# Performance work log

Hardware: AMD Instinct MI355X
Metric: run time of the kernel (lower is better)

Reference implementation:

```python
import jax, jax.numpy as jnp
import numpy as np

LEAK_RATE = 0.5
SPECTRAL_RADIUS = 0.9
T, IN_DIM, R_DIM, OUT_DIM = 32768, 128, 1024, 64


def setup_inputs() -> dict:
    key = jax.random.key(0)
    k1, k2, k3, k4 = jax.random.split(key, 4)
    input_data = jax.random.normal(k1, (T, IN_DIM), dtype=jnp.float32)
    # reservoir weights with spectral radius normalization (as in __init__)
    W = np.array(jax.random.normal(k2, (R_DIM, R_DIM), dtype=jnp.float32), dtype=np.float64)
    W *= SPECTRAL_RADIUS / np.max(np.abs(np.linalg.eigvals(W)))
    reservoir_weights = jnp.asarray(W, dtype=jnp.float32)
    input_weights = jax.random.normal(k3, (R_DIM, IN_DIM), dtype=jnp.float32)
    output_weights = jax.random.normal(k4, (R_DIM, OUT_DIM), dtype=jnp.float32) * 0.02
    return {
        "input_data": input_data,
        "input_weights": input_weights,
        "reservoir_weights": reservoir_weights,
        "output_weights": output_weights,
    }


def reference(input_data, input_weights, reservoir_weights, output_weights):
    a = jnp.float32(LEAK_RATE)
    # precompute input projection for all timesteps: [T, R]
    u = input_data @ input_weights.T

    def step(s, u_t):
        s_dec = (1.0 - a) * s                      # decayed previous state
        s_new = s_dec + a * jnp.tanh(u_t + reservoir_weights @ s_dec)
        return s_new, s_new

    s0 = jnp.zeros((reservoir_weights.shape[0],), dtype=input_data.dtype)
    _, states = jax.lax.scan(step, s0, u)          # states: [T, R]
    predictions = states @ output_weights          # [T, OUT_DIM]
    return predictions
```

## Files before the change

### kernel.cpp

```cpp
#include <hip/hip_runtime.h>
#include <math.h>


#define G_BLOCKS 32
#define ROWS     32
#define TPB      256
#define T_STEPS  32768
#define R_DIM    1024
#define IN_DIM   128
#define OUT_DIM  64

__global__ __launch_bounds__(TPB, 1)
void esn_scan_kernel(const float* __restrict__ x,
                     const float* __restrict__ Win,
                     const float* __restrict__ W,
                     const float* __restrict__ Wout,
                     float* __restrict__ out,
                     unsigned long long* __restrict__ sbuf)
{
    constexpr float A   = 0.5f;
    constexpr float DEC = 0.5f;

    const int b    = blockIdx.x;
    const int tid  = threadIdx.x;
    const int lane = tid & 63;
    const int wave = tid >> 6;
    const int r    = tid & 31;
    const int kg   = tid >> 5;

    __shared__ float s_dec[R_DIM];
    __shared__ float part[8][ROWS];
    __shared__ float u_lds[2][ROWS];
    __shared__ float s_new_lds[ROWS];
    __shared__ float x_lds[2][IN_DIM];
    __shared__ float win_lds[ROWS * 132];
    __shared__ float wout_lds[ROWS * OUT_DIM];

    float w[128];
    {
        const float* wrow = W + ((size_t)(b * ROWS + r)) * R_DIM + kg * 128;
        #pragma unroll
        for (int j = 0; j < 128; j += 4) {
            const float4 v = *(const float4*)(wrow + j);
            w[j] = v.x; w[j+1] = v.y; w[j+2] = v.z; w[j+3] = v.w;
        }
    }
    for (int i = tid; i < ROWS * IN_DIM; i += TPB) {
        int rr = i >> 7, cc = i & 127;
        win_lds[rr * 132 + cc] = Win[((size_t)(b * ROWS + rr)) * IN_DIM + cc];
    }
    for (int i = tid; i < ROWS * OUT_DIM; i += TPB)
        wout_lds[i] = Wout[(size_t)b * ROWS * OUT_DIM + i];
    for (int i = tid; i < R_DIM; i += TPB) s_dec[i] = 0.0f;
    if (tid < IN_DIM) {
        x_lds[0][tid] = x[tid];
        x_lds[1][tid] = x[IN_DIM + tid];
    }
    __syncthreads();

    if (wave == 1) {
        int rr = lane & 31, kh = lane >> 5;
        float acc = 0.f;
        const float* wl = &win_lds[rr * 132 + kh * 64];
        const float* xl = &x_lds[0][kh * 64];
        #pragma unroll
        for (int i = 0; i < 64; i += 4) {
            float4 wv = *(const float4*)(wl + i);
            float4 xv = *(const float4*)(xl + i);
            acc += wv.x*xv.x + wv.y*xv.y + wv.z*xv.z + wv.w*xv.w;
        }
        acc += __shfl_down(acc, 32);
        if (lane < 32) u_lds[0][rr] = acc;
    }
    __syncthreads();

    for (int t = 0; t < T_STEPS; ++t) {
        {
            float a0 = 0.f, a1 = 0.f, a2 = 0.f, a3 = 0.f;
            const float* sp = &s_dec[kg * 128];
            #pragma unroll
            for (int j = 0; j < 128; j += 4) {
                const float4 sv = *(const float4*)(sp + j);
                a0 += w[j]   * sv.x;
                a1 += w[j+1] * sv.y;
                a2 += w[j+2] * sv.z;
                a3 += w[j+3] * sv.w;
            }
            part[kg][r] = (a0 + a1) + (a2 + a3);
        }
        __syncthreads();

        if (wave == 0) {
            float snew = 0.f;
            if (lane < 32) {
                float tot = 0.f;
                #pragma unroll
                for (int k = 0; k < 8; ++k) tot += part[k][lane];
                const float y  = u_lds[t & 1][lane] + tot;
                const float sd = s_dec[b * ROWS + lane];
                snew = sd + A * tanhf(y);
                s_new_lds[lane] = snew;
                const unsigned long long pkt =
                    ((unsigned long long)(unsigned int)(t + 1) << 32)
                    | (unsigned long long)__float_as_uint(snew);
                __hip_atomic_store(&sbuf[(size_t)(t & 1) * R_DIM + b * ROWS + lane],
                                   pkt, __ATOMIC_RELAXED, __HIP_MEMORY_SCOPE_AGENT);
            }
        } else if (wave == 1 && t + 1 < T_STEPS) {
            const int tpre = (t + 2 < T_STEPS) ? (t + 2) : (T_STEPS - 1);
            const float xv0 = x[(size_t)tpre * IN_DIM + lane];
            const float xv1 = x[(size_t)tpre * IN_DIM + 64 + lane];
            int rr = lane & 31, kh = lane >> 5;
            float acc = 0.f;
            const float* wl = &win_lds[rr * 132 + kh * 64];
            const float* xl = &x_lds[(t + 1) & 1][kh * 64];
            #pragma unroll
            for (int i = 0; i < 64; i += 4) {
                float4 wv = *(const float4*)(wl + i);
                float4 xv = *(const float4*)(xl + i);
                acc += wv.x*xv.x + wv.y*xv.y + wv.z*xv.z + wv.w*xv.w;
            }
            acc += __shfl_down(acc, 32);
            if (lane < 32) u_lds[(t + 1) & 1][rr] = acc;
            x_lds[t & 1][lane]      = xv0;
            x_lds[t & 1][64 + lane] = xv1;
        }
        __syncthreads();

        if (wave == 2) {
            float acc = 0.f;
            #pragma unroll
            for (int rr = 0; rr < 32; ++rr)
                acc += s_new_lds[rr] * wout_lds[rr * OUT_DIM + lane];
            atomicAdd(&out[(size_t)t * OUT_DIM + lane], acc);
        }
        if (t + 1 < T_STEPS) {
            const int want = t + 1;
            unsigned long long v[4];
            const size_t base = (size_t)(t & 1) * R_DIM;
            #pragma unroll
            for (int j = 0; j < 4; ++j)
                v[j] = __hip_atomic_load(&sbuf[base + j * TPB + tid],
                                         __ATOMIC_RELAXED, __HIP_MEMORY_SCOPE_AGENT);
            bool ok;
            do {
                ok = true;
                #pragma unroll
                for (int j = 0; j < 4; ++j) {
                    if ((int)(v[j] >> 32) != want) {
                        ok = false;
                        __builtin_amdgcn_s_sleep(1);
                        v[j] = __hip_atomic_load(&sbuf[base + j * TPB + tid],
                                                 __ATOMIC_RELAXED,
                                                 __HIP_MEMORY_SCOPE_AGENT);
                    }
                }
            } while (!ok);
            #pragma unroll
            for (int j = 0; j < 4; ++j)
                s_dec[j * TPB + tid] = __uint_as_float((unsigned int)v[j]) * DEC;
        }
        __syncthreads();
    }
}

extern "C" void kernel_launch(void* const* d_in, const int* in_sizes, int n_in,
                              void* d_out, int out_size, void* d_ws, size_t ws_size,
                              hipStream_t stream) {
    const float* x    = (const float*)d_in[0];
    const float* Win  = (const float*)d_in[1];
    const float* W    = (const float*)d_in[2];
    const float* Wout = (const float*)d_in[3];
    float* out = (float*)d_out;
    unsigned long long* sbuf = (unsigned long long*)d_ws;

    hipMemsetAsync(d_out, 0, (size_t)out_size * sizeof(float), stream);

    esn_scan_kernel<<<G_BLOCKS, TPB, 0, stream>>>(x, Win, W, Wout, out, sbuf);
}
```

Baseline: 69.05 ms.

## Restructure ESN scan with packed 24-bit state exchange and separate output GEMM

Rewrites the recurrent scan so each thread computes four rows over a 32-wide k-slice, reduced with wave shuffles. The LDS partial-sum stage and one barrier per step go away. State exchange packs two 24-bit-truncated floats with an 8-bit tag into one 64-bit word, halving polling traffic. tanh uses an exp-based approximation, and the decay factor is folded into the weights. The per-step output projection with atomics is replaced by writing all states to workspace and running a separate tiled GEMM afterward. This trades state precision (24-bit mantissa truncation) and extra memory traffic for a shorter per-step critical path.

After: 135.6 ms. 96.4% more time.

```diff
diff --git a/kernel.cpp b/kernel.cpp
--- a/kernel.cpp
+++ b/kernel.cpp
@@ -3,165 +3,229 @@
 
 
 #define G_BLOCKS 32
-#define ROWS     32
 #define TPB      256
 #define T_STEPS  32768
 #define R_DIM    1024
 #define IN_DIM   128
 #define OUT_DIM  64
 
+__device__ __forceinline__ float tanh_fast(float y) {
+    float e = __expf(2.0f * y);
+    return 1.0f - 2.0f / (e + 1.0f);
+}
+
+__device__ __forceinline__ unsigned pack24(float v, unsigned tag) {
+    unsigned bts = __float_as_uint(v);
+    bts = (bts + 0x80u) >> 8;
+    return (tag << 24) | (bts & 0x00FFFFFFu);
+}
+__device__ __forceinline__ float unpack24(unsigned p) {
+    return __uint_as_float(p << 8);
+}
+
 __global__ __launch_bounds__(TPB, 1)
-void esn_scan_kernel(const float* __restrict__ x,
-                     const float* __restrict__ Win,
-                     const float* __restrict__ W,
-                     const float* __restrict__ Wout,
-                     float* __restrict__ out,
-                     unsigned long long* __restrict__ sbuf)
+void esn_scan(const float* __restrict__ x,
+              const float* __restrict__ Win,
+              const float* __restrict__ W,
+              float* __restrict__ states,
+              unsigned long long* __restrict__ sbuf)
 {
-    constexpr float A   = 0.5f;
-    constexpr float DEC = 0.5f;
-
+    constexpr float A = 0.5f, DEC = 0.5f;
     const int b    = blockIdx.x;
     const int tid  = threadIdx.x;
     const int lane = tid & 63;
     const int wave = tid >> 6;
-    const int r    = tid & 31;
-    const int kg   = tid >> 5;
-
-    __shared__ float s_dec[R_DIM];
-    __shared__ float part[8][ROWS];
-    __shared__ float u_lds[2][ROWS];
-    __shared__ float s_new_lds[ROWS];
+    const int c    = tid & 31;
+    const int rset = tid >> 5;
+    const bool is_pub = (c < 2);
+    const int lrow0 = rset * 4 + 2 * c;
+    const int grow0 = b * 32 + lrow0;
+    const int urow  = wave * 8 + (lane >> 3);
+    const int useg  = lane & 7;
+
+    __shared__ float win_lds[32 * 132];
     __shared__ float x_lds[2][IN_DIM];
-    __shared__ float win_lds[ROWS * 132];
-    __shared__ float wout_lds[ROWS * OUT_DIM];
-
-    float w[128];
+    __shared__ float u_lds[2][32];
+
+    float w0[32], w1[32], w2[32], w3[32];
     {
-        const float* wrow = W + ((size_t)(b * ROWS + r)) * R_DIM + kg * 128;
-        #pragma unroll
-        for (int j = 0; j < 128; j += 4) {
-            const float4 v = *(const float4*)(wrow + j);
-            w[j] = v.x; w[j+1] = v.y; w[j+2] = v.z; w[j+3] = v.w;
-        }
-    }
-    for (int i = tid; i < ROWS * IN_DIM; i += TPB) {
+        const float* base = W + (size_t)(b * 32 + rset * 4) * R_DIM + c * 32;
+        #pragma unroll
+        for (int k = 0; k < 32; k += 4) {
+            float4 v0 = *(const float4*)(base + 0 * R_DIM + k);
+            float4 v1 = *(const float4*)(base + 1 * R_DIM + k);
+            float4 v2 = *(const float4*)(base + 2 * R_DIM + k);
+            float4 v3 = *(const float4*)(base + 3 * R_DIM + k);
+            w0[k]=v0.x*DEC; w0[k+1]=v0.y*DEC; w0[k+2]=v0.z*DEC; w0[k+3]=v0.w*DEC;
+            w1[k]=v1.x*DEC; w1[k+1]=v1.y*DEC; w1[k+2]=v1.z*DEC; w1[k+3]=v1.w*DEC;
+            w2[k]=v2.x*DEC; w2[k+1]=v2.y*DEC; w2[k+2]=v2.z*DEC; w2[k+3]=v2.w*DEC;
+            w3[k]=v3.x*DEC; w3[k+1]=v3.y*DEC; w3[k+2]=v3.z*DEC; w3[k+3]=v3.w*DEC;
+        }
+    }
+    for (int i = tid; i < 32 * IN_DIM; i += TPB) {
         int rr = i >> 7, cc = i & 127;
-        win_lds[rr * 132 + cc] = Win[((size_t)(b * ROWS + rr)) * IN_DIM + cc];
-    }
-    for (int i = tid; i < ROWS * OUT_DIM; i += TPB)
-        wout_lds[i] = Wout[(size_t)b * ROWS * OUT_DIM + i];
-    for (int i = tid; i < R_DIM; i += TPB) s_dec[i] = 0.0f;
-    if (tid < IN_DIM) {
-        x_lds[0][tid] = x[tid];
-        x_lds[1][tid] = x[IN_DIM + tid];
+        win_lds[rr * 132 + cc] = Win[(size_t)(b * 32 + rr) * IN_DIM + cc];
+    }
+    float4 xr;
+    if (tid < 32) {
+        *(float4*)&x_lds[0][tid * 4] = *(const float4*)(x + tid * 4);
+        *(float4*)&x_lds[1][tid * 4] = *(const float4*)(x + IN_DIM + tid * 4);
+        xr = *(const float4*)(x + 2 * IN_DIM + tid * 4);
     }
     __syncthreads();
 
-    if (wave == 1) {
-        int rr = lane & 31, kh = lane >> 5;
-        float acc = 0.f;
-        const float* wl = &win_lds[rr * 132 + kh * 64];
-        const float* xl = &x_lds[0][kh * 64];
-        #pragma unroll
-        for (int i = 0; i < 64; i += 4) {
-            float4 wv = *(const float4*)(wl + i);
-            float4 xv = *(const float4*)(xl + i);
-            acc += wv.x*xv.x + wv.y*xv.y + wv.z*xv.z + wv.w*xv.w;
-        }
-        acc += __shfl_down(acc, 32);
-        if (lane < 32) u_lds[0][rr] = acc;
+    {
+        float up = 0.f;
+        const float* wl = &win_lds[urow * 132 + useg * 16];
+        const float* xl = &x_lds[0][useg * 16];
+        #pragma unroll
+        for (int j = 0; j < 16; j += 4) {
+            float4 wv = *(const float4*)(wl + j);
+            float4 xv = *(const float4*)(xl + j);
+            up += wv.x*xv.x + wv.y*xv.y + wv.z*xv.z + wv.w*xv.w;
+        }
+        up += __shfl_xor(up, 1, 64);
+        up += __shfl_xor(up, 2, 64);
+        up += __shfl_xor(up, 4, 64);
+        if (useg == 0) u_lds[0][urow] = up;
     }
     __syncthreads();
 
+    float s_prev0 = 0.f, s_prev1 = 0.f;
+    unsigned long long pub_pkt = 0;
+    float pub_s0 = 0.f, pub_s1 = 0.f;
+
     for (int t = 0; t < T_STEPS; ++t) {
+        if (t > 0 && is_pub) {
+            __hip_atomic_store(&sbuf[(size_t)(t & 1) * 512 + (grow0 >> 1)], pub_pkt,
+                               __ATOMIC_RELAXED, __HIP_MEMORY_SCOPE_AGENT);
+            *(float2*)&states[(size_t)(t - 1) * R_DIM + grow0] =
+                make_float2(pub_s0, pub_s1);
+        }
+        unsigned long long pk[16];
+        const unsigned long long* sb = sbuf + (size_t)(t & 1) * 512 + c * 16;
+        if (t > 0) {
+            #pragma unroll
+            for (int j = 0; j < 16; ++j)
+                pk[j] = __hip_atomic_load(sb + j, __ATOMIC_RELAXED,
+                                          __HIP_MEMORY_SCOPE_AGENT);
+        }
+        if (tid < 32) {
+            *(float4*)&x_lds[t & 1][tid * 4] = xr;
+            const int tn = (t + 3 < T_STEPS) ? (t + 3) : (T_STEPS - 1);
+            xr = *(const float4*)(x + (size_t)tn * IN_DIM + tid * 4);
+        }
         {
-            float a0 = 0.f, a1 = 0.f, a2 = 0.f, a3 = 0.f;
-            const float* sp = &s_dec[kg * 128];
-            #pragma unroll
-            for (int j = 0; j < 128; j += 4) {
-                const float4 sv = *(const float4*)(sp + j);
-                a0 += w[j]   * sv.x;
-                a1 += w[j+1] * sv.y;
-                a2 += w[j+2] * sv.z;
-                a3 += w[j+3] * sv.w;
+            float up = 0.f;
+            const float* wl = &win_lds[urow * 132 + useg * 16];
+            const float* xl = &x_lds[(t + 1) & 1][useg * 16];
+            #pragma unroll
+            for (int j = 0; j < 16; j += 4) {
+                float4 wv = *(const float4*)(wl + j);
+                float4 xv = *(const float4*)(xl + j);
+                up += wv.x*xv.x + wv.y*xv.y + wv.z*xv.z + wv.w*xv.w;
             }
-            part[kg][r] = (a0 + a1) + (a2 + a3);
+            up += __shfl_xor(up, 1, 64);
+            up += __shfl_xor(up, 2, 64);
+            up += __shfl_xor(up, 4, 64);
+            if (useg == 0) u_lds[(t + 1) & 1][urow] = up;
+        }
+        float sd[32];
+        if (t > 0) {
+            const unsigned tg = (unsigned)(t & 255);
+            int spins = 0;
+            while (true) {
+                bool ok = true;
+                #pragma unroll
+                for (int j = 0; j < 16; ++j) {
+                    unsigned lo = (unsigned)pk[j], hi = (unsigned)(pk[j] >> 32);
+                    ok &= ((lo >> 24) == tg) & ((hi >> 24) == tg);
+                }
+                if (ok) break;
+                if (++spins > 8) __builtin_amdgcn_s_sleep(1);
+                #pragma unroll
+                for (int j = 0; j < 16; ++j)
+                    pk[j] = __hip_atomic_load(sb + j, __ATOMIC_RELAXED,
+                                              __HIP_MEMORY_SCOPE_AGENT);
+            }
+            #pragma unroll
+            for (int j = 0; j < 16; ++j) {
+                sd[2 * j]     = unpack24((unsigned)pk[j]);
+                sd[2 * j + 1] = unpack24((unsigned)(pk[j] >> 32));
+            }
+        } else {
+            #pragma unroll
+            for (int k = 0; k < 32; ++k) sd[k] = 0.f;
+        }
+        float a0 = 0.f, a1 = 0.f, a2 = 0.f, a3 = 0.f;
+        #pragma unroll
+        for (int k = 0; k < 32; ++k) {
+            a0 += w0[k] * sd[k]; a1 += w1[k] * sd[k];
+            a2 += w2[k] * sd[k]; a3 += w3[k] * sd[k];
+        }
+        #pragma unroll
+        for (int m = 1; m <= 16; m <<= 1) {
+            a0 += __shfl_xor(a0, m, 64);
+            a1 += __shfl_xor(a1, m, 64);
+            a2 += __shfl_xor(a2, m, 64);
+            a3 += __shfl_xor(a3, m, 64);
+        }
+        if (is_pub) {
+            const float r0 = (c == 0) ? a0 : a2;
+            const float r1 = (c == 0) ? a1 : a3;
+            const float y0 = u_lds[t & 1][lrow0]     + r0;
+            const float y1 = u_lds[t & 1][lrow0 + 1] + r1;
+            const float s0 = DEC * s_prev0 + A * tanh_fast(y0);
+            const float s1 = DEC * s_prev1 + A * tanh_fast(y1);
+            s_prev0 = s0; s_prev1 = s1;
+            const unsigned tg1 = (unsigned)((t + 1) & 255);
+            pub_pkt = ((unsigned long long)pack24(s1, tg1) << 32) | pack24(s0, tg1);
+            pub_s0 = s0; pub_s1 = s1;
         }
         __syncthreads();
-
-        if (wave == 0) {
-            float snew = 0.f;
-            if (lane < 32) {
-                float tot = 0.f;
-                #pragma unroll
-                for (int k = 0; k < 8; ++k) tot += part[k][lane];
-                const float y  = u_lds[t & 1][lane] + tot;
-                const float sd = s_dec[b * ROWS + lane];
-                snew = sd + A * tanhf(y);
-                s_new_lds[lane] = snew;
-                const unsigned long long pkt =
-                    ((unsigned long long)(unsigned int)(t + 1) << 32)
-                    | (unsigned long long)__float_as_uint(snew);
-                __hip_atomic_store(&sbuf[(size_t)(t & 1) * R_DIM + b * ROWS + lane],
-                                   pkt, __ATOMIC_RELAXED, __HIP_MEMORY_SCOPE_AGENT);
-            }
-        } else if (wave == 1 && t + 1 < T_STEPS) {
-            const int tpre = (t + 2 < T_STEPS) ? (t + 2) : (T_STEPS - 1);
-            const float xv0 = x[(size_t)tpre * IN_DIM + lane];
-            const float xv1 = x[(size_t)tpre * IN_DIM + 64 + lane];
-            int rr = lane & 31, kh = lane >> 5;
-            float acc = 0.f;
-            const float* wl = &win_lds[rr * 132 + kh * 64];
-            const float* xl = &x_lds[(t + 1) & 1][kh * 64];
-            #pragma unroll
-            for (int i = 0; i < 64; i += 4) {
-                float4 wv = *(const float4*)(wl + i);
-                float4 xv = *(const float4*)(xl + i);
-                acc += wv.x*xv.x + wv.y*xv.y + wv.z*xv.z + wv.w*xv.w;
-            }
-            acc += __shfl_down(acc, 32);
-            if (lane < 32) u_lds[(t + 1) & 1][rr] = acc;
-            x_lds[t & 1][lane]      = xv0;
-            x_lds[t & 1][64 + lane] = xv1;
-        }
+    }
+    if (is_pub)
+        *(float2*)&states[(size_t)(T_STEPS - 1) * R_DIM + grow0] =
+            make_float2(pub_s0, pub_s1);
+}
+
+__global__ __launch_bounds__(256)
+void out_gemm(const float* __restrict__ states,
+              const float* __restrict__ Wout,
+              float* __restrict__ out)
+{
+    __shared__ float st[64][132];
+    __shared__ float wt[128][64];
+    const int t0  = blockIdx.x * 64;
+    const int tid = threadIdx.x;
+    const int tl  = tid >> 2;
+    const int cg  = tid & 3;
+    float acc[16];
+    #pragma unroll
+    for (int j = 0; j < 16; ++j) acc[j] = 0.f;
+
+    for (int kt = 0; kt < R_DIM; kt += 128) {
+        const float* src = states + (size_t)(t0 + tl) * R_DIM + kt + cg * 32;
+        #pragma unroll
+        for (int q = 0; q < 8; ++q)
+            *(float4*)&st[tl][cg * 32 + q * 4] = *(const float4*)(src + q * 4);
+        const float* wsrc = Wout + (size_t)(kt + (tid >> 1)) * OUT_DIM + (tid & 1) * 32;
+        #pragma unroll
+        for (int q = 0; q < 8; ++q)
+            *(float4*)&wt[tid >> 1][(tid & 1) * 32 + q * 4] = *(const float4*)(wsrc + q * 4);
         __syncthreads();
-
-        if (wave == 2) {
-            float acc = 0.f;
-            #pragma unroll
-            for (int rr = 0; rr < 32; ++rr)
-                acc += s_new_lds[rr] * wout_lds[rr * OUT_DIM + lane];
-            atomicAdd(&out[(size_t)t * OUT_DIM + lane], acc);
-        }
-        if (t + 1 < T_STEPS) {
-            const int want = t + 1;
-            unsigned long long v[4];
-            const size_t base = (size_t)(t & 1) * R_DIM;
-            #pragma unroll
-            for (int j = 0; j < 4; ++j)
-                v[j] = __hip_atomic_load(&sbuf[base + j * TPB + tid],
-                                         __ATOMIC_RELAXED, __HIP_MEMORY_SCOPE_AGENT);
-            bool ok;
-            do {
-                ok = true;
-                #pragma unroll
-                for (int j = 0; j < 4; ++j) {
-                    if ((int)(v[j] >> 32) != want) {
-                        ok = false;
-                        __builtin_amdgcn_s_sleep(1);
-                        v[j] = __hip_atomic_load(&sbuf[base + j * TPB + tid],
-                                                 __ATOMIC_RELAXED,
-                                                 __HIP_MEMORY_SCOPE_AGENT);
-                    }
-                }
-            } while (!ok);
-            #pragma unroll
-            for (int j = 0; j < 4; ++j)
-                s_dec[j * TPB + tid] = __uint_as_float((unsigned int)v[j]) * DEC;
+        #pragma unroll 4
+        for (int k = 0; k < 128; ++k) {
+            const float s = st[tl][k];
+            const float* wr = &wt[k][cg * 16];
+            #pragma unroll
+            for (int j = 0; j < 16; ++j) acc[j] += s * wr[j];
         }
         __syncthreads();
     }
+    float* op = out + (size_t)(t0 + tl) * OUT_DIM + cg * 16;
+    #pragma unroll
+    for (int q = 0; q < 4; ++q) *(float4*)(op + q * 4) = *(float4*)&acc[q * 4];
 }
 
 extern "C" void kernel_launch(void* const* d_in, const int* in_sizes, int n_in,
@@ -172,9 +236,10 @@
     const float* W    = (const float*)d_in[2];
     const float* Wout = (const float*)d_in[3];
     float* out = (float*)d_out;
+
     unsigned long long* sbuf = (unsigned long long*)d_ws;
-
-    hipMemsetAsync(d_out, 0, (size_t)out_size * sizeof(float), stream);
-
-    esn_scan_kernel<<<G_BLOCKS, TPB, 0, stream>>>(x, Win, W, Wout, out, sbuf);
-}
+    float* states = (float*)((char*)d_ws + 65536);
+
+    esn_scan<<<G_BLOCKS, TPB, 0, stream>>>(x, Win, W, states, sbuf);
+    out_gemm<<<T_STEPS / 64, 256, 0, stream>>>(states, Wout, out);
+}
```
